# Kernel optimization log

Hardware: AMD Instinct MI355X
Metric: run time of the kernel (lower is better)

The kernel has to match this reference:

```python
import jax, jax.numpy as jnp
import numpy as np

B, T, D, H = 4, 2048, 1024, 16
HS = D // H
EPS = 1e-5

def layer_norm(x, g, b):
    mu = jnp.mean(x, axis=-1, keepdims=True)
    var = jnp.var(x, axis=-1, keepdims=True)
    return (x - mu) * jax.lax.rsqrt(var + EPS) * g + b

def setup_inputs() -> dict:
    key = jax.random.key(0)
    ks = jax.random.split(key, 12)
    s_in = 1.0 / np.sqrt(D)
    s_ff = 1.0 / np.sqrt(4 * D)
    return {
        "x": jax.random.normal(ks[0], (B, T, D), jnp.float32),
        "Wq": jax.random.uniform(ks[1], (H, D, HS), jnp.float32, -s_in, s_in),
        "Wk": jax.random.uniform(ks[2], (H, D, HS), jnp.float32, -s_in, s_in),
        "Wv": jax.random.uniform(ks[3], (H, D, HS), jnp.float32, -s_in, s_in),
        "Wp": jax.random.uniform(ks[4], (D, D), jnp.float32, -s_in, s_in),
        "bp": jax.random.uniform(ks[5], (D,), jnp.float32, -s_in, s_in),
        "W1": jax.random.uniform(ks[6], (D, 4 * D), jnp.float32, -s_in, s_in),
        "b1": jax.random.uniform(ks[7], (4 * D,), jnp.float32, -s_in, s_in),
        "W2": jax.random.uniform(ks[8], (4 * D, D), jnp.float32, -s_ff, s_ff),
        "b2": jax.random.uniform(ks[9], (D,), jnp.float32, -s_ff, s_ff),
        "g1": jnp.ones((D,), jnp.float32),
        "be1": jnp.zeros((D,), jnp.float32),
        "g2": jnp.ones((D,), jnp.float32),
        "be2": jnp.zeros((D,), jnp.float32),
    }

def reference(x, Wq, Wk, Wv, Wp, bp, W1, b1, W2, b2, g1, be1, g2, be2):
    # pre-LN (note: residual uses the NORMALIZED tensor, matching original code)
    h = layer_norm(x, g1, be1)                          # [B,T,D]
    q = jnp.einsum('btd,hdk->bhtk', h, Wq)              # [B,H,T,hs]
    k = jnp.einsum('btd,hdk->bhtk', h, Wk)
    v = jnp.einsum('btd,hdk->bhtk', h, Wv)
    # NOTE: original scales by embedding_size**-0.5, not head_size
    scores = jnp.einsum('bhtk,bhsk->bhts', q, k) * (D ** -0.5)
    causal = jnp.tril(jnp.ones((T, T), bool))
    scores = jnp.where(causal, scores, -jnp.inf)
    att = jax.nn.softmax(scores, axis=-1)               # [B,H,T,T]
    o = jnp.einsum('bhts,bhsk->bhtk', att, v)
    o = o.transpose(0, 2, 1, 3).reshape(B, T, D)        # concat heads
    o = o @ Wp + bp
    x2 = h + o
    h2 = layer_norm(x2, g2, be2)
    ff = jax.nn.relu(h2 @ W1 + b1) @ W2 + b2
    return h2 + ff
```

## Files before the change

### kernel.cpp

```cpp
#include <hip/hip_runtime.h>
#include <hip/hip_bf16.h>

#define Bq 4
#define Tq 2048
#define Dq 1024
#define Hq 16
#define HSq 64
#define EPSq 1e-5f

typedef __attribute__((ext_vector_type(8))) short s16x8;
typedef __attribute__((ext_vector_type(4))) float f32x4;

#define GLL16(g, l)                                                        \
    __builtin_amdgcn_global_load_lds(                                      \
        (const __attribute__((address_space(1))) void*)(g),                \
        (__attribute__((address_space(3))) void*)(l), 16, 0, 0)

__device__ __forceinline__ ushort f2bf(float f) {
    union { float f; unsigned u; } x; x.f = f;
    unsigned r = x.u + 0x7fffu + ((x.u >> 16) & 1u);
    return (ushort)(r >> 16);
}

__global__ __launch_bounds__(256) void ln_bf16(const float* __restrict__ x,
                                               const float* __restrict__ g,
                                               const float* __restrict__ bb,
                                               float* __restrict__ y,
                                               ushort* __restrict__ y16) {
    __shared__ float sdata[8];
    int row = blockIdx.x;
    const float4* xr = (const float4*)(x + (size_t)row * Dq);
    float4 v = xr[threadIdx.x];
    float s  = v.x + v.y + v.z + v.w;
    float ss = v.x*v.x + v.y*v.y + v.z*v.z + v.w*v.w;
    for (int off = 32; off; off >>= 1) {
        s  += __shfl_down(s,  off);
        ss += __shfl_down(ss, off);
    }
    int lane = threadIdx.x & 63, wid = threadIdx.x >> 6;
    if (lane == 0) { sdata[wid] = s; sdata[4 + wid] = ss; }
    __syncthreads();
    if (threadIdx.x == 0) {
        sdata[0] = sdata[0] + sdata[1] + sdata[2] + sdata[3];
        sdata[4] = sdata[4] + sdata[5] + sdata[6] + sdata[7];
    }
    __syncthreads();
    float mu  = sdata[0] * (1.f / Dq);
    float var = sdata[4] * (1.f / Dq) - mu * mu;
    float inv = rsqrtf(var + EPSq);
    float4 gv = ((const float4*)g)[threadIdx.x];
    float4 bv = ((const float4*)bb)[threadIdx.x];
    float4 o;
    o.x = (v.x - mu) * inv * gv.x + bv.x;
    o.y = (v.y - mu) * inv * gv.y + bv.y;
    o.z = (v.z - mu) * inv * gv.z + bv.z;
    o.w = (v.w - mu) * inv * gv.w + bv.w;
    ((float4*)(y + (size_t)row * Dq))[threadIdx.x] = o;
    ushort4 u4;
    u4.x = f2bf(o.x); u4.y = f2bf(o.y); u4.z = f2bf(o.z); u4.w = f2bf(o.w);
    *(ushort4*)(y16 + (size_t)row * Dq + threadIdx.x * 4) = u4;
}

__global__ __launch_bounds__(256) void repack_qkvT(const float* __restrict__ Wqm,
                                                   const float* __restrict__ Wkm,
                                                   const float* __restrict__ Wvm,
                                                   ushort* __restrict__ out) {
    __shared__ float tile[64][65];
    int bid = blockIdx.x;
    int p  = bid >> 8;
    int hh = (bid >> 4) & 15;
    int kt = bid & 15;
    int k0 = kt * 64;
    const float* W = (p == 0) ? Wqm : ((p == 1) ? Wkm : Wvm);
    float scale = (p == 0) ? 0.03125f : 1.0f;
    int j  = threadIdx.x & 63;
    int i0 = threadIdx.x >> 6;
#pragma unroll
    for (int r = 0; r < 16; r++) {
        int i = r * 4 + i0;
        tile[i][j] = W[(size_t)hh * (Dq * HSq) + (size_t)(k0 + i) * HSq + j];
    }
    __syncthreads();
#pragma unroll
    for (int r = 0; r < 16; r++) {
        int i = r * 4 + i0;
        out[(size_t)(p * Dq + hh * HSq + i) * Dq + k0 + j] = f2bf(tile[j][i] * scale);
    }
}

__global__ __launch_bounds__(256) void transpose_cvt(const float* __restrict__ in,
                                                     ushort* __restrict__ out,
                                                     int K, int N) {
    __shared__ float tile[64][65];
    int k0 = blockIdx.y * 64, n0 = blockIdx.x * 64;
    int j  = threadIdx.x & 63;
    int i0 = threadIdx.x >> 6;
#pragma unroll
    for (int r = 0; r < 16; r++) {
        int i = r * 4 + i0;
        tile[i][j] = in[(size_t)(k0 + i) * N + n0 + j];
    }
    __syncthreads();
#pragma unroll
    for (int r = 0; r < 16; r++) {
        int i = r * 4 + i0;
        out[(size_t)(n0 + i) * K + k0 + j] = f2bf(tile[j][i]);
    }
}

__global__ __launch_bounds__(256) void gemm_bf16(const ushort* __restrict__ A,
                                                 const ushort* __restrict__ BT,
                                                 const float* __restrict__ bias,
                                                 const float* __restrict__ resid,
                                                 void* __restrict__ Cp,
                                                 ushort* __restrict__ vtg,
                                                 int M, int N, int K,
                                                 int lda, int ldc,
                                                 int relu, int out_bf16) {
    __shared__ ushort As[128 * 32];
    __shared__ ushort Bs[128 * 32];
    int tid = threadIdx.x;
    int row0 = blockIdx.y * 128, col0 = blockIdx.x * 128;
    int w = tid >> 6, lane = tid & 63;
    int wy = w >> 1, wx = w & 1;
    int lm = lane & 15, quad = lane >> 4;

    f32x4 zero = {0.f, 0.f, 0.f, 0.f};
    f32x4 acc[4][4];
#pragma unroll
    for (int i = 0; i < 4; i++)
#pragma unroll
        for (int j = 0; j < 4; j++) acc[i][j] = zero;

    int srow = lane >> 2;
    int scol = (lane & 3) * 8;
    const ushort* Ag0 = A  + (size_t)(row0 + w * 32 + srow) * lda + scol;
    const ushort* Ag1 = A  + (size_t)(row0 + w * 32 + 16 + srow) * lda + scol;
    const ushort* Bg0 = BT + (size_t)(col0 + w * 32 + srow) * K + scol;
    const ushort* Bg1 = BT + (size_t)(col0 + w * 32 + 16 + srow) * K + scol;
    ushort* Al0 = &As[(w * 32) * 32];
    ushort* Al1 = &As[(w * 32 + 16) * 32];
    ushort* Bl0 = &Bs[(w * 32) * 32];
    ushort* Bl1 = &Bs[(w * 32 + 16) * 32];

    for (int k0 = 0; k0 < K; k0 += 32) {
        __syncthreads();
        GLL16(Ag0 + k0, Al0);
        GLL16(Ag1 + k0, Al1);
        GLL16(Bg0 + k0, Bl0);
        GLL16(Bg1 + k0, Bl1);
        __syncthreads();
        s16x8 af[4], bf_[4];
#pragma unroll
        for (int t = 0; t < 4; t++) {
            af[t]  = *(const s16x8*)&As[(wy * 64 + t * 16 + lm) * 32 + quad * 8];
            bf_[t] = *(const s16x8*)&Bs[(wx * 64 + t * 16 + lm) * 32 + quad * 8];
        }
#pragma unroll
        for (int i = 0; i < 4; i++)
#pragma unroll
            for (int j = 0; j < 4; j++)
                acc[i][j] = __builtin_amdgcn_mfma_f32_16x16x32_bf16(af[i], bf_[j], acc[i][j], 0, 0, 0);
    }

    if (vtg && col0 >= 2048) {
#pragma unroll
        for (int ti = 0; ti < 4; ti++) {
            int r0 = row0 + wy * 64 + ti * 16 + quad * 4;
            int bb = r0 >> 11;
            int t  = r0 & (Tq - 1);
#pragma unroll
            for (int tj = 0; tj < 4; tj++) {
                int hsg = col0 - 2048 + wx * 64 + tj * 16 + lm;
                ushort4 u;
                u.x = f2bf(acc[ti][tj][0]);
                u.y = f2bf(acc[ti][tj][1]);
                u.z = f2bf(acc[ti][tj][2]);
                u.w = f2bf(acc[ti][tj][3]);
                *(ushort4*)(vtg + ((size_t)(bb * Hq + (hsg >> 6)) * HSq + (hsg & 63)) * Tq + t) = u;
            }
        }
        return;
    }

    float bcol[4];
#pragma unroll
    for (int tj = 0; tj < 4; tj++)
        bcol[tj] = bias ? bias[col0 + wx * 64 + tj * 16 + lm] : 0.f;

#pragma unroll
    for (int ti = 0; ti < 4; ti++) {
#pragma unroll
        for (int p = 0; p < 4; p++) {
            int r = row0 + wy * 64 + ti * 16 + quad * 4 + p;
#pragma unroll
            for (int tj = 0; tj < 4; tj++) {
                int c = col0 + wx * 64 + tj * 16 + lm;
                float v = acc[ti][tj][p] + bcol[tj];
                if (relu) v = fmaxf(v, 0.f);
                if (resid) v += resid[(size_t)r * ldc + c];
                if (out_bf16) ((ushort*)Cp)[(size_t)r * ldc + c] = f2bf(v);
                else          ((float*)Cp)[(size_t)r * ldc + c] = v;
            }
        }
    }
}

__global__ __launch_bounds__(256) void attn_mfma(const ushort* __restrict__ qkv,
                                                 const ushort* __restrict__ VtG,
                                                 ushort* __restrict__ o16) {
    __shared__ ushort Ks[64 * 72];
    __shared__ ushort Vt[64 * 64];
    __shared__ ushort Ps[4 * 16 * 72];

    int gid = blockIdx.x;
    int b  = gid >> 8;
    int hh = (gid >> 4) & 15;
    int pr = (gid + 7 * b) & 15;
    int qa = pr;
    int qb = 31 - pr;

    int tid = threadIdx.x;
    int w = tid >> 6, lane = tid & 63;
    int lm = lane & 15, quad = lane >> 4;

    const int rs3 = 3 * Dq;
    const ushort* qbase = qkv + (size_t)(b * Tq) * rs3 + hh * HSq;
    int qra = qa * 64 + w * 16 + lm;
    int qrb = qb * 64 + w * 16 + lm;
    s16x8 aqa0 = *(const s16x8*)(qbase + (size_t)qra * rs3 + quad * 8);
    s16x8 aqa1 = *(const s16x8*)(qbase + (size_t)qra * rs3 + 32 + quad * 8);
    s16x8 aqb0 = *(const s16x8*)(qbase + (size_t)qrb * rs3 + quad * 8);
    s16x8 aqb1 = *(const s16x8*)(qbase + (size_t)qrb * rs3 + 32 + quad * 8);

    s16x8 ones;
#pragma unroll
    for (int j = 0; j < 8; j++) ones[j] = (short)0x3F80;

    f32x4 zero = {0.f, 0.f, 0.f, 0.f};
    f32x4 oa[4], ob[4];
#pragma unroll
    for (int nt = 0; nt < 4; nt++) { oa[nt] = zero; ob[nt] = zero; }
    f32x4 la = zero, lb = zero;

    const ushort* kbase = qkv + (size_t)(b * Tq) * rs3 + Dq + hh * HSq;
    const ushort* vtb = VtG + (size_t)((b * Hq + hh) * HSq) * Tq;

    int kr = tid >> 3, kc = (tid & 7) * 8;
    int vh = tid >> 2, vc0 = (tid & 3) * 8;
    int vswz = (((vh >> 3) ^ vh) & 7) << 3;

    s16x8 kp0 = *(const s16x8*)(kbase + (size_t)kr * rs3 + kc);
    s16x8 kp1 = *(const s16x8*)(kbase + (size_t)(kr + 32) * rs3 + kc);
    s16x8 vp0 = *(const s16x8*)(vtb + (size_t)vh * Tq + vc0);
    s16x8 vp1 = *(const s16x8*)(vtb + (size_t)vh * Tq + vc0 + 32);

    auto do_tile = [&](const s16x8& aq0, const s16x8& aq1,
                       f32x4 (&o_acc)[4], f32x4& l_acc, int diag) {
        f32x4 sacc[4];
#pragma unroll
        for (int kt2 = 0; kt2 < 4; kt2++) {
            const ushort* krp = &Ks[(kt2 * 16 + lm) * 72 + quad * 8];
            s16x8 bk0 = *(const s16x8*)krp;
            s16x8 bk1 = *(const s16x8*)(krp + 32);
            f32x4 t = __builtin_amdgcn_mfma_f32_16x16x32_bf16(aq0, bk0, zero, 0, 0, 0);
            sacc[kt2] = __builtin_amdgcn_mfma_f32_16x16x32_bf16(aq1, bk1, t, 0, 0, 0);
        }
        if (diag) {
#pragma unroll
            for (int kt2 = 0; kt2 < 4; kt2++)
#pragma unroll
                for (int r = 0; r < 4; r++)
                    if (kt2 * 16 + lm > w * 16 + quad * 4 + r) sacc[kt2][r] = -1e30f;
        }
#pragma unroll
        for (int kt2 = 0; kt2 < 4; kt2++)
#pragma unroll
            for (int r = 0; r < 4; r++)
                Ps[(w * 16 + quad * 4 + r) * 72 + kt2 * 16 + lm] = f2bf(__expf(sacc[kt2][r]));

        s16x8 ap0 = *(const s16x8*)&Ps[(w * 16 + lm) * 72 + quad * 8];
        s16x8 ap1 = *(const s16x8*)&Ps[(w * 16 + lm) * 72 + 32 + quad * 8];

#pragma unroll
        for (int nt = 0; nt < 4; nt++) {
            int n = nt * 16 + lm;
            int swz = (((n >> 3) ^ n) & 7) << 3;
            s16x8 bv0 = *(const s16x8*)&Vt[n * 64 + ((quad * 8) ^ swz)];
            s16x8 bv1 = *(const s16x8*)&Vt[n * 64 + ((32 + quad * 8) ^ swz)];
            f32x4 t = __builtin_amdgcn_mfma_f32_16x16x32_bf16(ap0, bv0, o_acc[nt], 0, 0, 0);
            o_acc[nt] = __builtin_amdgcn_mfma_f32_16x16x32_bf16(ap1, bv1, t, 0, 0, 0);
        }
        f32x4 t2 = __builtin_amdgcn_mfma_f32_16x16x32_bf16(ap0, ones, l_acc, 0, 0, 0);
        l_acc = __builtin_amdgcn_mfma_f32_16x16x32_bf16(ap1, ones, t2, 0, 0, 0);
    };

    for (int kt = 0; kt <= qb; kt++) {
        __syncthreads();
        *(s16x8*)&Ks[kr * 72 + kc] = kp0;
        *(s16x8*)&Ks[(kr + 32) * 72 + kc] = kp1;
        *(s16x8*)&Vt[vh * 64 + (vc0 ^ vswz)] = vp0;
        *(s16x8*)&Vt[vh * 64 + ((vc0 + 32) ^ vswz)] = vp1;
        __syncthreads();

        if (kt < qb) {
            const ushort* kb = kbase + (size_t)((kt + 1) * 64) * rs3;
            kp0 = *(const s16x8*)(kb + (size_t)kr * rs3 + kc);
            kp1 = *(const s16x8*)(kb + (size_t)(kr + 32) * rs3 + kc);
            const ushort* vb = vtb + (size_t)vh * Tq + (kt + 1) * 64;
            vp0 = *(const s16x8*)(vb + vc0);
            vp1 = *(const s16x8*)(vb + vc0 + 32);
        }

        do_tile(aqb0, aqb1, ob, lb, kt == qb);
        if (kt <= qa)
            do_tile(aqa0, aqa1, oa, la, kt == qa);
    }

#pragma unroll
    for (int r = 0; r < 4; r++) {
        float inva = 1.f / la[r];
        float invb = 1.f / lb[r];
        size_t rowa = (size_t)(b * Tq + qa * 64 + w * 16 + quad * 4 + r);
        size_t rowb = (size_t)(b * Tq + qb * 64 + w * 16 + quad * 4 + r);
#pragma unroll
        for (int nt = 0; nt < 4; nt++) {
            o16[rowa * Dq + hh * HSq + nt * 16 + lm] = f2bf(oa[nt][r] * inva);
            o16[rowb * Dq + hh * HSq + nt * 16 + lm] = f2bf(ob[nt][r] * invb);
        }
    }
}

extern "C" void kernel_launch(void* const* d_in, const int* in_sizes, int n_in,
                              void* d_out, int out_size, void* d_ws, size_t ws_size,
                              hipStream_t stream) {
    const float* x   = (const float*)d_in[0];
    const float* Wq  = (const float*)d_in[1];
    const float* Wk  = (const float*)d_in[2];
    const float* Wv  = (const float*)d_in[3];
    const float* Wp  = (const float*)d_in[4];
    const float* bp  = (const float*)d_in[5];
    const float* W1  = (const float*)d_in[6];
    const float* b1  = (const float*)d_in[7];
    const float* W2  = (const float*)d_in[8];
    const float* b2  = (const float*)d_in[9];
    const float* g1  = (const float*)d_in[10];
    const float* be1 = (const float*)d_in[11];
    const float* g2  = (const float*)d_in[12];
    const float* be2 = (const float*)d_in[13];
    float* out = (float*)d_out;

    const size_t MB = 1u << 20;
    char* ws = (char*)d_ws;
    float*  slotA = (float*)(ws);
    ushort* qkv   = (ushort*)(ws + 32 * MB);
    float*  pbuf  = (float*)(ws + 32 * MB);
    ushort* u16   = (ushort*)(ws + 32 * MB);
    ushort* slotC = (ushort*)(ws + 96 * MB);
    ushort* WqkvT = (ushort*)(ws + 112 * MB);
    ushort* WpT   = (ushort*)(ws + 118 * MB);
    ushort* W1T   = (ushort*)(ws + 120 * MB);
    ushort* W2T   = (ushort*)(ws + 128 * MB);
    ushort* VtG   = (ushort*)(ws + 136 * MB);

    const int rows = Bq * Tq;

    hipLaunchKernelGGL(repack_qkvT, dim3(3 * 16 * 16), dim3(256), 0, stream, Wq, Wk, Wv, WqkvT);
    hipLaunchKernelGGL(transpose_cvt, dim3(Dq / 64, Dq / 64), dim3(256), 0, stream, Wp, WpT, Dq, Dq);
    hipLaunchKernelGGL(transpose_cvt, dim3(4 * Dq / 64, Dq / 64), dim3(256), 0, stream, W1, W1T, Dq, 4 * Dq);
    hipLaunchKernelGGL(transpose_cvt, dim3(Dq / 64, 4 * Dq / 64), dim3(256), 0, stream, W2, W2T, 4 * Dq, Dq);

    hipLaunchKernelGGL(ln_bf16, dim3(rows), dim3(256), 0, stream, x, g1, be1, slotA, slotC);
    hipLaunchKernelGGL(gemm_bf16, dim3(3 * Dq / 128, rows / 128), dim3(256), 0, stream,
                       slotC, WqkvT, (const float*)nullptr, (const float*)nullptr, (void*)qkv, VtG,
                       rows, 3 * Dq, Dq, Dq, 3 * Dq, 0, 1);
    hipLaunchKernelGGL(attn_mfma, dim3(Bq * Hq * 16), dim3(256), 0, stream, qkv, VtG, slotC);
    hipLaunchKernelGGL(gemm_bf16, dim3(Dq / 128, rows / 128), dim3(256), 0, stream,
                       slotC, WpT, bp, slotA, (void*)pbuf, (ushort*)nullptr,
                       rows, Dq, Dq, Dq, Dq, 0, 0);
    hipLaunchKernelGGL(ln_bf16, dim3(rows), dim3(256), 0, stream, pbuf, g2, be2, slotA, slotC);
    hipLaunchKernelGGL(gemm_bf16, dim3(4 * Dq / 128, rows / 128), dim3(256), 0, stream,
                       slotC, W1T, b1, (const float*)nullptr, (void*)u16, (ushort*)nullptr,
                       rows, 4 * Dq, Dq, Dq, 4 * Dq, 1, 1);
    hipLaunchKernelGGL(gemm_bf16, dim3(Dq / 128, rows / 128), dim3(256), 0, stream,
                       u16, W2T, b2, slotA, (void*)out, (ushort*)nullptr,
                       rows, Dq, 4 * Dq, 4 * Dq, Dq, 0, 0);
}
```

Before: 587.1 us.

## Replace GEMM with multi-stage pipelined 128x256 tile kernel using swizzled LDS

Replaces the simple single-buffered 128x128 bf16 MFMA GEMM with a 512-thread kernel that computes 128x256 tiles over K=64 steps. A and B tiles are double- and triple-buffered in LDS through direct global-to-LDS loads. The LDS layout is XOR-swizzled to avoid bank conflicts. Phase barriers, s_setprio and explicit vmcnt waits are meant to overlap memory loads with MFMA work. A 1D grid with an XCD-aware block remap is meant to improve L2 locality across chiplets, at the cost of higher LDS use and more complex synchronisation.

```diff
diff --git a/kernel.cpp b/kernel.cpp
--- a/kernel.cpp
+++ b/kernel.cpp
@@ -15,6 +15,10 @@
     __builtin_amdgcn_global_load_lds(                                      \
         (const __attribute__((address_space(1))) void*)(g),                \
         (__attribute__((address_space(3))) void*)(l), 16, 0, 0)
+
+#define PH_BAR() do { __builtin_amdgcn_sched_barrier(0);                   \
+                      __builtin_amdgcn_s_barrier();                        \
+                      __builtin_amdgcn_sched_barrier(0); } while (0)
 
 __device__ __forceinline__ ushort f2bf(float f) {
     union { float f; unsigned u; } x; x.f = f;
@@ -108,75 +112,143 @@
     }
 }
 
-__global__ __launch_bounds__(256) void gemm_bf16(const ushort* __restrict__ A,
-                                                 const ushort* __restrict__ BT,
-                                                 const float* __restrict__ bias,
-                                                 const float* __restrict__ resid,
-                                                 void* __restrict__ Cp,
-                                                 ushort* __restrict__ vtg,
-                                                 int M, int N, int K,
-                                                 int lda, int ldc,
-                                                 int relu, int out_bf16) {
-    __shared__ ushort As[128 * 32];
-    __shared__ ushort Bs[128 * 32];
+__global__ __launch_bounds__(512, 2) void gemm_mp(const ushort* __restrict__ A,
+                                                  const ushort* __restrict__ BT,
+                                                  const float* __restrict__ bias,
+                                                  const float* __restrict__ resid,
+                                                  void* __restrict__ Cp,
+                                                  ushort* __restrict__ vtg,
+                                                  int M, int N, int K,
+                                                  int lda, int ldc,
+                                                  int relu, int out_bf16) {
+    __shared__ ushort lds[2 * 8192 + 3 * 16384];
+    ushort* Alds = lds;
+    ushort* Blds = lds + 2 * 8192;
+
     int tid = threadIdx.x;
-    int row0 = blockIdx.y * 128, col0 = blockIdx.x * 128;
     int w = tid >> 6, lane = tid & 63;
-    int wy = w >> 1, wx = w & 1;
     int lm = lane & 15, quad = lane >> 4;
+    int wm = w >> 2, wn = w & 3;
+
+    int nwg = gridDim.x;
+    int bid = blockIdx.x;
+    int wk = bid;
+    if ((nwg & 7) == 0) { int cpx = nwg >> 3; wk = (bid & 7) * cpx + (bid >> 3); }
+    int mtiles = M >> 7;
+    int rt = wk % mtiles, ct = wk / mtiles;
+    int row0 = rt << 7, col0 = ct << 8;
+
+    int cswz = (lane & 7) ^ (lane >> 3);
+    int srow = w * 8 + (lane >> 3);
+    const ushort* pA = A  + (size_t)(row0 + srow) * lda + cswz * 8;
+    const ushort* pB = BT + (size_t)(col0 + srow) * K  + cswz * 8;
+
+    auto stageA = [&](int slot, int t) {
+        const ushort* g = pA + (size_t)t * 64;
+        ushort* l = Alds + slot * 8192 + w * 512;
+        GLL16(g, l);
+        GLL16(g + (size_t)64 * lda, l + 4096);
+    };
+    auto stageB = [&](int slot, int t, int h) {
+        const ushort* g = pB + (size_t)t * 64 + (size_t)(h * 128) * K;
+        ushort* l = Blds + slot * 16384 + h * 8192 + w * 512;
+        GLL16(g, l);
+        GLL16(g + (size_t)64 * K, l + 4096);
+    };
+
+    int swq0 = (quad * 8) ^ ((lm & 7) << 3);
+    int swq1 = (32 + quad * 8) ^ ((lm & 7) << 3);
 
     f32x4 zero = {0.f, 0.f, 0.f, 0.f};
     f32x4 acc[4][4];
 #pragma unroll
     for (int i = 0; i < 4; i++)
 #pragma unroll
-        for (int j = 0; j < 4; j++) acc[i][j] = zero;
-
-    int srow = lane >> 2;
-    int scol = (lane & 3) * 8;
-    const ushort* Ag0 = A  + (size_t)(row0 + w * 32 + srow) * lda + scol;
-    const ushort* Ag1 = A  + (size_t)(row0 + w * 32 + 16 + srow) * lda + scol;
-    const ushort* Bg0 = BT + (size_t)(col0 + w * 32 + srow) * K + scol;
-    const ushort* Bg1 = BT + (size_t)(col0 + w * 32 + 16 + srow) * K + scol;
-    ushort* Al0 = &As[(w * 32) * 32];
-    ushort* Al1 = &As[(w * 32 + 16) * 32];
-    ushort* Bl0 = &Bs[(w * 32) * 32];
-    ushort* Bl1 = &Bs[(w * 32 + 16) * 32];
-
-    for (int k0 = 0; k0 < K; k0 += 32) {
-        __syncthreads();
-        GLL16(Ag0 + k0, Al0);
-        GLL16(Ag1 + k0, Al1);
-        GLL16(Bg0 + k0, Bl0);
-        GLL16(Bg1 + k0, Bl1);
-        __syncthreads();
-        s16x8 af[4], bf_[4];
-#pragma unroll
-        for (int t = 0; t < 4; t++) {
-            af[t]  = *(const s16x8*)&As[(wy * 64 + t * 16 + lm) * 32 + quad * 8];
-            bf_[t] = *(const s16x8*)&Bs[(wx * 64 + t * 16 + lm) * 32 + quad * 8];
-        }
-#pragma unroll
-        for (int i = 0; i < 4; i++)
-#pragma unroll
-            for (int j = 0; j < 4; j++)
-                acc[i][j] = __builtin_amdgcn_mfma_f32_16x16x32_bf16(af[i], bf_[j], acc[i][j], 0, 0, 0);
+        for (int jj = 0; jj < 4; jj++) acc[i][jj] = zero;
+
+    int nkt = K >> 6;
+
+    stageA(0, 0);
+    stageB(0, 0, 0); stageB(0, 0, 1);
+    stageB(1, 1, 0); stageB(1, 1, 1);
+    __builtin_amdgcn_sched_barrier(0);
+    asm volatile("s_waitcnt vmcnt(4)" ::: "memory");
+    __builtin_amdgcn_s_barrier();
+    __builtin_amdgcn_sched_barrier(0);
+
+    int sA = 0, sB = 0;
+    for (int t = 0; t < nkt; ++t) {
+        const bool stA = (t + 1 < nkt);
+        const bool stB = (t + 2 < nkt);
+        int sB2 = sB + 2; if (sB2 >= 3) sB2 -= 3;
+        const ushort* Ab = Alds + sA * 8192  + (wm * 64 + lm) * 64;
+        const ushort* Bb = Blds + sB * 16384 + (wn * 64 + lm) * 64;
+        s16x8 a[4][2], b0[2][2], b1[2][2];
+
+#pragma unroll
+        for (int m = 0; m < 4; m++) {
+            a[m][0] = *(const s16x8*)(Ab + m * 1024 + swq0);
+            a[m][1] = *(const s16x8*)(Ab + m * 1024 + swq1);
+        }
+#pragma unroll
+        for (int nf = 0; nf < 2; nf++) {
+            b0[nf][0] = *(const s16x8*)(Bb + nf * 1024 + swq0);
+            b0[nf][1] = *(const s16x8*)(Bb + nf * 1024 + swq1);
+        }
+        if (stA) stageA(sA ^ 1, t + 1);
+        if (stB) stageB(sB2, t + 2, 0);
+        PH_BAR();
+        __builtin_amdgcn_s_setprio(1);
+#pragma unroll
+        for (int m = 0; m < 4; m++)
+#pragma unroll
+            for (int nf = 0; nf < 2; nf++) {
+                f32x4 tt = __builtin_amdgcn_mfma_f32_16x16x32_bf16(a[m][0], b0[nf][0], acc[m][nf], 0, 0, 0);
+                acc[m][nf] = __builtin_amdgcn_mfma_f32_16x16x32_bf16(a[m][1], b0[nf][1], tt, 0, 0, 0);
+            }
+        __builtin_amdgcn_s_setprio(0);
+        PH_BAR();
+
+#pragma unroll
+        for (int nf = 0; nf < 2; nf++) {
+            b1[nf][0] = *(const s16x8*)(Bb + (nf + 2) * 1024 + swq0);
+            b1[nf][1] = *(const s16x8*)(Bb + (nf + 2) * 1024 + swq1);
+        }
+        if (stB) stageB(sB2, t + 2, 1);
+        PH_BAR();
+        __builtin_amdgcn_s_setprio(1);
+#pragma unroll
+        for (int m = 0; m < 4; m++)
+#pragma unroll
+            for (int nf = 0; nf < 2; nf++) {
+                f32x4 tt = __builtin_amdgcn_mfma_f32_16x16x32_bf16(a[m][0], b1[nf][0], acc[m][nf + 2], 0, 0, 0);
+                acc[m][nf + 2] = __builtin_amdgcn_mfma_f32_16x16x32_bf16(a[m][1], b1[nf][1], tt, 0, 0, 0);
+            }
+        __builtin_amdgcn_s_setprio(0);
+        __builtin_amdgcn_sched_barrier(0);
+        if (stB)      { asm volatile("s_waitcnt vmcnt(4)" ::: "memory"); }
+        else if (stA) { asm volatile("s_waitcnt vmcnt(0)" ::: "memory"); }
+        __builtin_amdgcn_s_barrier();
+        __builtin_amdgcn_sched_barrier(0);
+
+        sA ^= 1;
+        sB += 1; if (sB >= 3) sB -= 3;
     }
 
     if (vtg && col0 >= 2048) {
 #pragma unroll
-        for (int ti = 0; ti < 4; ti++) {
-            int r0 = row0 + wy * 64 + ti * 16 + quad * 4;
+        for (int m = 0; m < 4; m++) {
+            int r0 = row0 + wm * 64 + m * 16 + quad * 4;
             int bb = r0 >> 11;
             int t  = r0 & (Tq - 1);
 #pragma unroll
-            for (int tj = 0; tj < 4; tj++) {
-                int hsg = col0 - 2048 + wx * 64 + tj * 16 + lm;
+            for (int nf = 0; nf < 4; nf++) {
+                int hsg = col0 - 2048 + wn * 64 + nf * 16 + lm;
                 ushort4 u;
-                u.x = f2bf(acc[ti][tj][0]);
-                u.y = f2bf(acc[ti][tj][1]);
-                u.z = f2bf(acc[ti][tj][2]);
-                u.w = f2bf(acc[ti][tj][3]);
+                u.x = f2bf(acc[m][nf][0]);
+                u.y = f2bf(acc[m][nf][1]);
+                u.z = f2bf(acc[m][nf][2]);
+                u.w = f2bf(acc[m][nf][3]);
                 *(ushort4*)(vtg + ((size_t)(bb * Hq + (hsg >> 6)) * HSq + (hsg & 63)) * Tq + t) = u;
             }
         }
@@ -185,18 +257,18 @@
 
     float bcol[4];
 #pragma unroll
-    for (int tj = 0; tj < 4; tj++)
-        bcol[tj] = bias ? bias[col0 + wx * 64 + tj * 16 + lm] : 0.f;
-
-#pragma unroll
-    for (int ti = 0; ti < 4; ti++) {
+    for (int nf = 0; nf < 4; nf++)
+        bcol[nf] = bias ? bias[col0 + wn * 64 + nf * 16 + lm] : 0.f;
+
+#pragma unroll
+    for (int m = 0; m < 4; m++) {
 #pragma unroll
         for (int p = 0; p < 4; p++) {
-            int r = row0 + wy * 64 + ti * 16 + quad * 4 + p;
-#pragma unroll
-            for (int tj = 0; tj < 4; tj++) {
-                int c = col0 + wx * 64 + tj * 16 + lm;
-                float v = acc[ti][tj][p] + bcol[tj];
+            int r = row0 + wm * 64 + m * 16 + quad * 4 + p;
+#pragma unroll
+            for (int nf = 0; nf < 4; nf++) {
+                int c = col0 + wn * 64 + nf * 16 + lm;
+                float v = acc[m][nf][p] + bcol[nf];
                 if (relu) v = fmaxf(v, 0.f);
                 if (resid) v += resid[(size_t)r * ldc + c];
                 if (out_bf16) ((ushort*)Cp)[(size_t)r * ldc + c] = f2bf(v);
@@ -371,18 +443,18 @@
     hipLaunchKernelGGL(transpose_cvt, dim3(Dq / 64, 4 * Dq / 64), dim3(256), 0, stream, W2, W2T, 4 * Dq, Dq);
 
     hipLaunchKernelGGL(ln_bf16, dim3(rows), dim3(256), 0, stream, x, g1, be1, slotA, slotC);
-    hipLaunchKernelGGL(gemm_bf16, dim3(3 * Dq / 128, rows / 128), dim3(256), 0, stream,
+    hipLaunchKernelGGL(gemm_mp, dim3((rows / 128) * (3 * Dq / 256)), dim3(512), 0, stream,
                        slotC, WqkvT, (const float*)nullptr, (const float*)nullptr, (void*)qkv, VtG,
                        rows, 3 * Dq, Dq, Dq, 3 * Dq, 0, 1);
     hipLaunchKernelGGL(attn_mfma, dim3(Bq * Hq * 16), dim3(256), 0, stream, qkv, VtG, slotC);
-    hipLaunchKernelGGL(gemm_bf16, dim3(Dq / 128, rows / 128), dim3(256), 0, stream,
+    hipLaunchKernelGGL(gemm_mp, dim3((rows / 128) * (Dq / 256)), dim3(512), 0, stream,
                        slotC, WpT, bp, slotA, (void*)pbuf, (ushort*)nullptr,
                        rows, Dq, Dq, Dq, Dq, 0, 0);
     hipLaunchKernelGGL(ln_bf16, dim3(rows), dim3(256), 0, stream, pbuf, g2, be2, slotA, slotC);
-    hipLaunchKernelGGL(gemm_bf16, dim3(4 * Dq / 128, rows / 128), dim3(256), 0, stream,
+    hipLaunchKernelGGL(gemm_mp, dim3((rows / 128) * (4 * Dq / 256)), dim3(512), 0, stream,
                        slotC, W1T, b1, (const float*)nullptr, (void*)u16, (ushort*)nullptr,
                        rows, 4 * Dq, Dq, Dq, 4 * Dq, 1, 1);
-    hipLaunchKernelGGL(gemm_bf16, dim3(Dq / 128, rows / 128), dim3(256), 0, stream,
+    hipLaunchKernelGGL(gemm_mp, dim3((rows / 128) * (Dq / 256)), dim3(512), 0, stream,
                        u16, W2T, b2, slotA, (void*)out, (ushort*)nullptr,
                        rows, Dq, 4 * Dq, 4 * Dq, Dq, 0, 0);
 }
```

Measured after the change: 529.2 us. 9.9% less time.
